# Performance work log

Hardware: AMD Instinct MI355X
Metric: run time of the kernel (lower is better)

Reference implementation:

```python
import jax, jax.numpy as jnp
import numpy as np

B, L, F = 4, 8192, 1024
H, D = 16, 64
EPS = 1e-6

def _phi(x):
    # ELU+1 positive feature map, standard for linear attention
    return jax.nn.elu(x) + 1.0

def setup_inputs() -> dict:
    key = jax.random.key(0)
    ks = jax.random.split(key, 6)
    s_in = 1.0
    s_w = 1.0 / np.sqrt(F)
    s_o = 1.0 / np.sqrt(H * D)
    return {
        "inputs_q": jax.random.normal(ks[0], (B, L, F), jnp.float32),
        "inputs_kv": jax.random.normal(ks[1], (B, L, F), jnp.float32),
        "Wq": jax.random.normal(ks[2], (F, H, D), jnp.float32) * s_w,
        "Wk": jax.random.normal(ks[3], (F, H, D), jnp.float32) * s_w,
        "Wv": jax.random.normal(ks[4], (F, H, D), jnp.float32) * s_w,
        "Wo": jax.random.normal(ks[5], (H, D, F), jnp.float32) * s_o,
    }

def reference(inputs_q, inputs_kv, Wq, Wk, Wv, Wo):
    # QKV projections (split-head kernels, no bias)
    q = jnp.einsum('bqf,fhd->bqhd', inputs_q, Wq)   # [B,Lq,H,D]
    k = jnp.einsum('bkf,fhd->bkhd', inputs_kv, Wk)  # [B,Lk,H,D]
    v = jnp.einsum('bkf,fhd->bkhd', inputs_kv, Wv)  # [B,Lk,H,D]

    qp = _phi(q)
    kp = _phi(k)

    # Linear attention: O = phi(q) @ (phi(k)^T V) / (phi(q) . sum_k phi(k))
    kv = jnp.einsum('bkhd,bkhe->bhde', kp, v)       # [B,H,D,D] small state
    ksum = jnp.sum(kp, axis=1)                       # [B,H,D]
    z = 1.0 / (jnp.einsum('bqhd,bhd->bqh', qp, ksum) + EPS)
    out = jnp.einsum('bqhd,bhde,bqh->bqhe', qp, kv, z)  # [B,Lq,H,D]

    # Output projection
    return jnp.einsum('bqhe,hef->bqf', out, Wo)      # [B,Lq,F]
```

## Files before the change

### kernel.cpp

```cpp
#include <hip/hip_runtime.h>
#include <hip/hip_fp16.h>
#include <math.h>

typedef _Float16 half8  __attribute__((ext_vector_type(8)));
typedef _Float16 half4v __attribute__((ext_vector_type(4)));
typedef float    floatx4 __attribute__((ext_vector_type(4)));

#define NB   4
#define LL   8192
#define FF   1024
#define HH   16
#define DD   64
#define MTOT 32768
#define KK   1024
#define NN   1024
#define ZSCALE 65536.0f

__device__ __forceinline__ void gload_lds16(const void* g, void* l) {
  __builtin_amdgcn_global_load_lds(
      (const __attribute__((address_space(1))) void*)g,
      (__attribute__((address_space(3))) void*)l, 16, 0, 0);
}

__device__ __forceinline__ float phi_act(float x) {
  return x > 0.f ? x + 1.f : __expf(x);
}

__global__ void k_cvt2(const float* __restrict__ a, const float* __restrict__ b,
                       _Float16* __restrict__ da, _Float16* __restrict__ db, int n4each) {
  int stride = gridDim.x * blockDim.x;
  for (int i = blockIdx.x * blockDim.x + threadIdx.x; i < 2 * n4each; i += stride) {
    const float* s; _Float16* d; int j;
    if (i < n4each) { s = a; d = da; j = i; }
    else            { s = b; d = db; j = i - n4each; }
    float4 v = reinterpret_cast<const float4*>(s)[j];
    half4v h;
    h[0] = (_Float16)v.x; h[1] = (_Float16)v.y; h[2] = (_Float16)v.z; h[3] = (_Float16)v.w;
    reinterpret_cast<half4v*>(d)[j] = h;
  }
}

__global__ void k_cvt(const float* __restrict__ src, _Float16* __restrict__ dst, int n4) {
  int stride = gridDim.x * blockDim.x;
  for (int i = blockIdx.x * blockDim.x + threadIdx.x; i < n4; i += stride) {
    float4 v = reinterpret_cast<const float4*>(src)[i];
    half4v h;
    h[0] = (_Float16)v.x; h[1] = (_Float16)v.y; h[2] = (_Float16)v.z; h[3] = (_Float16)v.w;
    reinterpret_cast<half4v*>(dst)[i] = h;
  }
}

__global__ void k_cvt_t(const float* __restrict__ W0, const float* __restrict__ W1,
                        const float* __restrict__ W2,
                        _Float16* __restrict__ T0, _Float16* __restrict__ T1,
                        _Float16* __restrict__ T2) {
  __shared__ float tile[32][33];
  int bid = blockIdx.x;
  int w = bid >> 10, rem = bid & 1023;
  int ti = rem >> 5, tj = rem & 31;
  const float* src = (w == 0) ? W0 : (w == 1) ? W1 : W2;
  _Float16*    dst = (w == 0) ? T0 : (w == 1) ? T1 : T2;
  int t = threadIdx.x;
  int r = t >> 3, c4 = (t & 7) << 2;
  float4 v = *reinterpret_cast<const float4*>(&src[(size_t)(ti * 32 + r) * FF + tj * 32 + c4]);
  tile[r][c4 + 0] = v.x; tile[r][c4 + 1] = v.y; tile[r][c4 + 2] = v.z; tile[r][c4 + 3] = v.w;
  __syncthreads();
  half4v h;
  h[0] = (_Float16)tile[c4 + 0][r];
  h[1] = (_Float16)tile[c4 + 1][r];
  h[2] = (_Float16)tile[c4 + 2][r];
  h[3] = (_Float16)tile[c4 + 3][r];
  *reinterpret_cast<half4v*>(&dst[(size_t)(tj * 32 + r) * FF + ti * 32 + c4]) = h;
}


template<int MATB, int HALF>
__device__ __forceinline__ void stage_half(const _Float16* __restrict__ G, int row0,
                                           int col0, _Float16* plane, int tid) {
  #pragma unroll
  for (int is = 0; is < 2; ++is) {
    int lin = is * 8192 + tid * 16;
    int swz = lin ^ (((lin >> 7) & 7) << 4);
    int rp = swz >> 7;
    int kb = swz & 127;
    int row;
    if constexpr (MATB) row = (rp >> 5) * 64 + HALF * 32 + (rp & 31);
    else                row = (rp >> 6) * 128 + HALF * 64 + (rp & 63);
    gload_lds16(G + (size_t)(row0 + row) * 1024 + col0 + (kb >> 1),
                (char*)plane + lin);
  }
}

__device__ __forceinline__ half8 frag_read(const _Float16* plane, int rp, int kk, int lh) {
  int byte = rp * 128 + kk * 64 + lh * 16;
  byte ^= ((byte >> 7) & 7) << 4;
  return *(const half8*)((const char*)plane + byte);
}

template<int MH, int NH>
__device__ __forceinline__ void qreads(const _Float16* sm, int buf,
                                       half8 (&bA)[8], half8 (&bB)[2][4],
                                       int wr, int wc, int lr, int lh) {
  if constexpr (NH == 0) {
    const _Float16* Ap = sm + buf * 32768 + MH * 8192;
    #pragma unroll
    for (int m = 0; m < 4; ++m)
      #pragma unroll
      for (int kk = 0; kk < 2; ++kk)
        bA[m * 2 + kk] = frag_read(Ap, wr * 64 + m * 16 + lr, kk, lh);
  }
  if constexpr (MH == 0) {
    const _Float16* Bp = sm + buf * 32768 + 16384 + NH * 8192;
    #pragma unroll
    for (int n = 0; n < 2; ++n)
      #pragma unroll
      for (int kk = 0; kk < 2; ++kk)
        bB[NH][n * 2 + kk] = frag_read(Bp, wc * 32 + n * 16 + lr, kk, lh);
  }
}

template<int MH, int NH, bool VM4>
__device__ __forceinline__ void qmfma(half8 (&bA)[8], half8 (&bB)[2][4],
                                      floatx4 (&acc)[8][4]) {
  if constexpr (VM4) {
    asm volatile("s_waitcnt vmcnt(4)" ::: "memory");
  }
  __builtin_amdgcn_s_barrier();
  __builtin_amdgcn_s_setprio(1);
  #pragma unroll
  for (int m = 0; m < 4; ++m)
    #pragma unroll
    for (int n = 0; n < 2; ++n)
      #pragma unroll
      for (int kk = 0; kk < 2; ++kk)
        acc[MH * 4 + m][NH * 2 + n] = __builtin_amdgcn_mfma_f32_16x16x32_f16(
            bA[m * 2 + kk], bB[NH][n * 2 + kk], acc[MH * 4 + m][NH * 2 + n], 0, 0, 0);
  __builtin_amdgcn_s_setprio(0);
  __builtin_amdgcn_s_barrier();
}

template<int TBUF>
__device__ __forceinline__ void do_tile(int t, const _Float16* __restrict__ Ab,
                                        const _Float16* __restrict__ Bb,
                                        int i0, int j0, _Float16* sm, int tid,
                                        half8 (&bA)[8], half8 (&bB)[2][4],
                                        floatx4 (&acc)[8][4],
                                        int wr, int wc, int lr, int lh) {
  _Float16* self  = sm + TBUF * 32768;
  _Float16* other = sm + (TBUF ^ 1) * 32768;
  const int c1 = ((t + 1 < 16) ? (t + 1) : 15) * 64;
  const int c2 = ((t + 2 < 16) ? (t + 2) : 15) * 64;
  qreads<0, 0>(sm, TBUF, bA, bB, wr, wc, lr, lh);
  stage_half<1, 1>(Bb, j0, c1, other + 24576, tid);
  qmfma<0, 0, false>(bA, bB, acc);
  qreads<0, 1>(sm, TBUF, bA, bB, wr, wc, lr, lh);
  stage_half<0, 1>(Ab, i0, c1, other + 8192, tid);
  qmfma<0, 1, false>(bA, bB, acc);
  qreads<1, 0>(sm, TBUF, bA, bB, wr, wc, lr, lh);
  stage_half<0, 0>(Ab, i0, c2, self + 0, tid);
  qmfma<1, 0, false>(bA, bB, acc);
  stage_half<1, 0>(Bb, j0, c2, self + 16384, tid);
  qmfma<1, 1, true>(bA, bB, acc);
}

template<int MODE, bool PHI>
__global__ __launch_bounds__(512, 2)
void k_gemm(const _Float16* __restrict__ A, const _Float16* __restrict__ BT,
            void* __restrict__ Cptr, float* __restrict__ aux, float outScale) {
  __shared__ __align__(16) _Float16 smem[65536];
  const int tid  = threadIdx.x;
  const int lane = tid & 63;
  const int wid  = tid >> 6;
  const int wr = wid >> 2, wc = wid & 3;
  const int lr = lane & 15, lh = lane >> 4;

  constexpr int NT = (MODE == 1) ? 8 : 4;
  constexpr int CH = (MODE == 1) ? 128 : 64;
  const int tile = (blockIdx.x & 7) * CH + (blockIdx.x >> 3);
  const int tm = tile / NT, tn = tile % NT;
  const int i0 = tm * 256, j0 = tn * 256;

  const _Float16* Ab = A;
  const _Float16* Bb = (MODE == 2) ? BT + ((size_t)(i0 >> 13)) * ((size_t)NN * KK) : BT;

  floatx4 acc[8][4];
  #pragma unroll
  for (int m = 0; m < 8; ++m)
    #pragma unroll
    for (int n = 0; n < 4; ++n)
      #pragma unroll
      for (int r = 0; r < 4; ++r) acc[m][n][r] = 0.f;

  _Float16* sm = (_Float16*)smem;
  half8 bA[8];
  half8 bB[2][4];

  stage_half<0, 0>(Ab, i0, 0,  sm + 0,             tid);
  stage_half<1, 0>(Bb, j0, 0,  sm + 16384,         tid);
  stage_half<1, 1>(Bb, j0, 0,  sm + 24576,         tid);
  stage_half<0, 1>(Ab, i0, 0,  sm + 8192,          tid);
  stage_half<0, 0>(Ab, i0, 64, sm + 32768 + 0,     tid);
  stage_half<1, 0>(Bb, j0, 64, sm + 32768 + 16384, tid);
  asm volatile("s_waitcnt vmcnt(4)" ::: "memory");
  __builtin_amdgcn_s_barrier();

  #pragma unroll 1
  for (int tt = 0; tt < 8; ++tt) {
    do_tile<0>(2 * tt,     Ab, Bb, i0, j0, sm, tid, bA, bB, acc, wr, wc, lr, lh);
    do_tile<1>(2 * tt + 1, Ab, Bb, i0, j0, sm, tid, bA, bB, acc, wr, wc, lr, lh);
  }

  asm volatile("s_waitcnt vmcnt(0)" ::: "memory");
  __builtin_amdgcn_s_barrier();

  if constexpr (MODE == 0) {
    _Float16* C = (_Float16*)Cptr;
    const int bq = i0 >> 13;
    float ks[4];
    #pragma unroll
    for (int n = 0; n < 4; ++n)
      ks[n] = aux[(size_t)bq * 1024 + j0 + wc * 64 + n * 16 + lr];
    #pragma unroll
    for (int m = 0; m < 8; ++m) {
      int row = i0 + wr * 128 + m * 16 + lh * 4;
      #pragma unroll
      for (int r = 0; r < 4; ++r) {
        float p[4];
        float dot = 0.f;
        #pragma unroll
        for (int n = 0; n < 4; ++n) {
          p[n] = phi_act(acc[m][n][r]);
          dot = fmaf(p[n], ks[n], dot);
        }
        dot += __shfl_xor(dot, 1);
        dot += __shfl_xor(dot, 2);
        dot += __shfl_xor(dot, 4);
        dot += __shfl_xor(dot, 8);
        float zf = ZSCALE / (dot + 1e-6f);
        #pragma unroll
        for (int n = 0; n < 4; ++n)
          C[(size_t)(row + r) * NN + j0 + wc * 64 + n * 16 + lr] = (_Float16)(p[n] * zf);
      }
    }
  } else if constexpr (MODE == 2) {
    float* C = (float*)Cptr;
    #pragma unroll
    for (int m = 0; m < 8; ++m) {
      int row = i0 + wr * 128 + m * 16 + lh * 4;
      #pragma unroll
      for (int n = 0; n < 4; ++n) {
        int col = j0 + wc * 64 + n * 16 + lr;
        #pragma unroll
        for (int r = 0; r < 4; ++r)
          C[(size_t)(row + r) * NN + col] = acc[m][n][r] * outScale;
      }
    }
  } else {
    const int seg = j0 >> 10;
    const int j0s = j0 & 1023;
    const int bb  = i0 >> 13;
    const int l0  = i0 & 8191;
    float s[4] = {0.f, 0.f, 0.f, 0.f};
    #pragma unroll
    for (int m = 0; m < 8; ++m) {
      int l0l = wr * 128 + m * 16 + lh * 4;
      #pragma unroll
      for (int n = 0; n < 4; ++n) {
        int n_loc = wc * 64 + n * 16 + lr;
        int byte = (n_loc * 512 + l0l * 2) ^ ((n_loc & 7) << 4);
        half4v h;
        #pragma unroll
        for (int r = 0; r < 4; ++r) {
          float v = acc[m][n][r];
          if (seg == 0) { v = phi_act(v); s[n] += v; }
          h[r] = (_Float16)v;
        }
        *(half4v*)((char*)sm + byte) = h;
      }
    }
    if (seg == 0) {
      #pragma unroll
      for (int n = 0; n < 4; ++n) {
        s[n] += __shfl_xor(s[n], 16);
        s[n] += __shfl_xor(s[n], 32);
      }
      if (lh == 0) {
        int ch = (l0 >> 7) + wr;
        size_t base = ((size_t)bb * 64 + ch) * 1024 + j0s + wc * 64 + lr;
        #pragma unroll
        for (int n = 0; n < 4; ++n) aux[base + n * 16] = s[n];
      }
    }
    __syncthreads();
    _Float16* C = (_Float16*)Cptr;
    const size_t nbase = ((size_t)seg * 4 + bb) * 1024 + j0s;
    #pragma unroll 1
    for (int pass = 0; pass < 16; ++pass) {
      int n_loc = pass * 16 + (tid >> 5);
      int lo = (tid & 31) * 16;
      int byte = (n_loc * 512 + lo) ^ ((n_loc & 7) << 4);
      half8 v = *(const half8*)((char*)sm + byte);
      *(half8*)&C[(nbase + n_loc) * LL + l0 + (lo >> 1)] = v;
    }
  }
}

__global__ void k_ksum_red(const float* __restrict__ part, float* __restrict__ ksum) {
  int i = blockIdx.x * 256 + threadIdx.x;
  int b = i >> 10, col = i & 1023;
  float s = 0.f;
  for (int c = 0; c < 64; ++c) s += part[((size_t)b * 64 + c) * 1024 + col];
  ksum[i] = s;
}

__global__ __launch_bounds__(64)
void k_stageB(const _Float16* __restrict__ kpT, const _Float16* __restrict__ vT,
              float* __restrict__ kvpart) {
  __shared__ _Float16 Ak[64 * 72];
  __shared__ _Float16 Bv[64 * 72];
  const int bid = blockIdx.x;
  const int bh = bid >> 4, cc = bid & 15;
  const int lane = threadIdx.x;
  const int lr = lane & 15, lh = lane >> 4;
  const _Float16* Ab = kpT + (size_t)bh * 64 * LL + cc * 512;
  const _Float16* Bb = vT  + (size_t)bh * 64 * LL + cc * 512;

  floatx4 acc[4][4];
  #pragma unroll
  for (int m = 0; m < 4; ++m)
    #pragma unroll
    for (int n = 0; n < 4; ++n)
      #pragma unroll
      for (int r = 0; r < 4; ++r) acc[m][n][r] = 0.f;

  for (int kt = 0; kt < 512; kt += 64) {
    __syncthreads();
    #pragma unroll
    for (int j = 0; j < 8; ++j) {
      int chunk = lane + 64 * j;
      int rr = chunk >> 3;
      int off = (chunk & 7) * 8;
      *(half8*)&Ak[rr * 72 + off] = *(const half8*)&Ab[(size_t)rr * LL + kt + off];
      *(half8*)&Bv[rr * 72 + off] = *(const half8*)&Bb[(size_t)rr * LL + kt + off];
    }
    __syncthreads();
    #pragma unroll
    for (int ks = 0; ks < 2; ++ks) {
      half8 af[4], bf[4];
      #pragma unroll
      for (int m = 0; m < 4; ++m) af[m] = *(const half8*)&Ak[(m * 16 + lr) * 72 + ks * 32 + lh * 8];
      #pragma unroll
      for (int n = 0; n < 4; ++n) bf[n] = *(const half8*)&Bv[(n * 16 + lr) * 72 + ks * 32 + lh * 8];
      #pragma unroll
      for (int m = 0; m < 4; ++m)
        #pragma unroll
        for (int n = 0; n < 4; ++n)
          acc[m][n] = __builtin_amdgcn_mfma_f32_16x16x32_f16(af[m], bf[n], acc[m][n], 0, 0, 0);
    }
  }
  float* op = kvpart + (size_t)bid * 4096;
  #pragma unroll
  for (int m = 0; m < 4; ++m)
    #pragma unroll
    for (int n = 0; n < 4; ++n)
      #pragma unroll
      for (int r = 0; r < 4; ++r)
        op[(m * 16 + lh * 4 + r) * 64 + n * 16 + lr] = acc[m][n][r];
}

__global__ void k_reduce_kv(const float* __restrict__ kvpart, float* __restrict__ kv) {
  int gid = blockIdx.x * 256 + threadIdx.x;
  int bh = gid >> 12, i = gid & 4095;
  float s = 0.f;
  for (int c = 0; c < 16; ++c) s += kvpart[((size_t)bh * 16 + c) * 4096 + i];
  kv[gid] = s;
}

__global__ __launch_bounds__(256)
void k_mker(const float* __restrict__ kv, const _Float16* __restrict__ Wo16,
            _Float16* __restrict__ MT) {
  __shared__ float kvs[4096];
  int bid = blockIdx.x;
  int fc = bid & 3, h = (bid >> 2) & 15, b = bid >> 6;
  const float* kvp = kv + ((size_t)b * 16 + h) * 4096;
  for (int i = threadIdx.x; i < 4096; i += 256) kvs[i] = kvp[i];
  __syncthreads();
  int f = fc * 256 + threadIdx.x;
  float acc[64];
  #pragma unroll
  for (int d = 0; d < 64; ++d) acc[d] = 0.f;
  for (int e = 0; e < 64; ++e) {
    float wv = (float)Wo16[(size_t)(h * 64 + e) * 1024 + f];
    #pragma unroll
    for (int d = 0; d < 64; ++d) acc[d] = fmaf(kvs[d * 64 + e], wv, acc[d]);
  }
  _Float16* op = MT + ((size_t)b * 1024 + f) * 1024 + h * 64;
  #pragma unroll
  for (int g = 0; g < 8; ++g) {
    half8 o;
    #pragma unroll
    for (int j = 0; j < 8; ++j) o[j] = (_Float16)acc[g * 8 + j];
    *(half8*)&op[g * 8] = o;
  }
}

extern "C" void kernel_launch(void* const* d_in, const int* in_sizes, int n_in,
                              void* d_out, int out_size, void* d_ws, size_t ws_size,
                              hipStream_t stream) {
  (void)in_sizes; (void)n_in; (void)out_size; (void)ws_size;
  const float* xq  = (const float*)d_in[0];
  const float* xkv = (const float*)d_in[1];
  const float* Wq  = (const float*)d_in[2];
  const float* Wk  = (const float*)d_in[3];
  const float* Wv  = (const float*)d_in[4];
  const float* Wo  = (const float*)d_in[5];

  char* ws = (char*)d_ws;
  _Float16* qp16 = (_Float16*)(ws + 0);
  _Float16* kpT  = (_Float16*)(ws + 67108864);
  _Float16* vT   = (_Float16*)(ws + 134217728);
  _Float16* WqT  = (_Float16*)(ws + 201326592);
  _Float16* WkT  = (_Float16*)(ws + 203423744);
  _Float16* WvT  = (_Float16*)(ws + 205520896);
  _Float16* Wo16 = (_Float16*)(ws + 207618048);
  float*    ksum = (float*)(ws + 209715200);
  float*    kv   = (float*)(ws + 209731584);
  float*    kvpart = (float*)(ws + 210780160);
  float*    ksum_part = (float*)(ws + 210780160);
  _Float16* MT   = (_Float16*)(ws + 227557376);

  _Float16* Xq16  = (_Float16*)d_out;
  _Float16* Xkv16 = Xq16 + 33554432;

  k_cvt2<<<4096, 256, 0, stream>>>(xq, xkv, Xq16, Xkv16, 8388608);
  k_cvt<<<512,  256, 0, stream>>>(Wo, Wo16, 262144);
  k_cvt_t<<<3072, 256, 0, stream>>>(Wq, Wk, Wv, WqT, WkT, WvT);

  k_gemm<1, false><<<1024, 512, 0, stream>>>(Xkv16, WkT, kpT, ksum_part, 1.0f);
  k_ksum_red<<<16, 256, 0, stream>>>(ksum_part, ksum);

  k_stageB<<<1024, 64, 0, stream>>>(kpT, vT, kvpart);
  k_reduce_kv<<<1024, 256, 0, stream>>>(kvpart, kv);
  k_mker<<<256, 256, 0, stream>>>(kv, Wo16, MT);

  k_gemm<0, true><<<512, 512, 0, stream>>>(Xq16, WqT, qp16, ksum, 1.0f);

  k_gemm<2, false><<<512, 512, 0, stream>>>(qp16, MT, d_out, nullptr, 1.0f / ZSCALE);
}
```

Baseline: 462.6 us.

## Fuse phi(K)^T V state computation into the KV projection GEMM epilogue

The transposed K and V weights are interleaved per head so that each 256-column GEMM tile holds phi(K) and V for two heads. The epilogue then computes per-tile partial kv states with MFMA directly from LDS, which removes the kpT/vT intermediate writes (128 MB of fp16) and the separate k_stageB kernel. The cost is more partial states to reduce (32 chunks instead of 16) and extra epilogue work and register pressure in the large GEMM.

```diff
diff --git a/kernel.cpp b/kernel.cpp
--- a/kernel.cpp
+++ b/kernel.cpp
@@ -52,14 +52,12 @@
 
 __global__ void k_cvt_t(const float* __restrict__ W0, const float* __restrict__ W1,
                         const float* __restrict__ W2,
-                        _Float16* __restrict__ T0, _Float16* __restrict__ T1,
-                        _Float16* __restrict__ T2) {
+                        _Float16* __restrict__ T0, _Float16* __restrict__ TKV) {
   __shared__ float tile[32][33];
   int bid = blockIdx.x;
   int w = bid >> 10, rem = bid & 1023;
   int ti = rem >> 5, tj = rem & 31;
   const float* src = (w == 0) ? W0 : (w == 1) ? W1 : W2;
-  _Float16*    dst = (w == 0) ? T0 : (w == 1) ? T1 : T2;
   int t = threadIdx.x;
   int r = t >> 3, c4 = (t & 7) << 2;
   float4 v = *reinterpret_cast<const float4*>(&src[(size_t)(ti * 32 + r) * FF + tj * 32 + c4]);
@@ -70,7 +68,11 @@
   h[1] = (_Float16)tile[c4 + 1][r];
   h[2] = (_Float16)tile[c4 + 2][r];
   h[3] = (_Float16)tile[c4 + 3][r];
-  *reinterpret_cast<half4v*>(&dst[(size_t)(tj * 32 + r) * FF + ti * 32 + c4]) = h;
+  int n = tj * 32 + r;
+  _Float16* dst; size_t orow;
+  if (w == 0) { dst = T0;  orow = n; }
+  else        { dst = TKV; orow = (size_t)(n >> 6) * 128 + (n & 63) + (w == 2 ? 64 : 0); }
+  *reinterpret_cast<half4v*>(&dst[orow * FF + ti * 32 + c4]) = h;
 }
 
 
@@ -166,7 +168,8 @@
 template<int MODE, bool PHI>
 __global__ __launch_bounds__(512, 2)
 void k_gemm(const _Float16* __restrict__ A, const _Float16* __restrict__ BT,
-            void* __restrict__ Cptr, float* __restrict__ aux, float outScale) {
+            void* __restrict__ Cptr, float* __restrict__ aux, float* __restrict__ aux2,
+            float outScale) {
   __shared__ __align__(16) _Float16 smem[65536];
   const int tid  = threadIdx.x;
   const int lane = tid & 63;
@@ -256,10 +259,10 @@
       }
     }
   } else {
-    const int seg = j0 >> 10;
-    const int j0s = j0 & 1023;
-    const int bb  = i0 >> 13;
-    const int l0  = i0 & 8191;
+    const int b  = i0 >> 13;
+    const int l0 = i0 & 8191;
+    const int isK = !(wc & 1);
+    const int hh  = tn * 2 + (wc >> 1);
     float s[4] = {0.f, 0.f, 0.f, 0.f};
     #pragma unroll
     for (int m = 0; m < 8; ++m) {
@@ -272,13 +275,13 @@
         #pragma unroll
         for (int r = 0; r < 4; ++r) {
           float v = acc[m][n][r];
-          if (seg == 0) { v = phi_act(v); s[n] += v; }
+          if (isK) { v = phi_act(v); s[n] += v; }
           h[r] = (_Float16)v;
         }
         *(half4v*)((char*)sm + byte) = h;
       }
     }
-    if (seg == 0) {
+    if (isK) {
       #pragma unroll
       for (int n = 0; n < 4; ++n) {
         s[n] += __shfl_xor(s[n], 16);
@@ -286,22 +289,52 @@
       }
       if (lh == 0) {
         int ch = (l0 >> 7) + wr;
-        size_t base = ((size_t)bb * 64 + ch) * 1024 + j0s + wc * 64 + lr;
+        size_t base = ((size_t)b * 64 + ch) * 1024 + (size_t)hh * 64 + lr;
         #pragma unroll
         for (int n = 0; n < 4; ++n) aux[base + n * 16] = s[n];
       }
     }
     __syncthreads();
-    _Float16* C = (_Float16*)Cptr;
-    const size_t nbase = ((size_t)seg * 4 + bb) * 1024 + j0s;
+    const int khd = wid >> 2;
+    const int db = ((wid >> 1) & 1) * 32, eb = (wid & 1) * 32;
+    const int hb = khd * 128;
+    floatx4 a2[2][2];
+    #pragma unroll
+    for (int md = 0; md < 2; ++md)
+      #pragma unroll
+      for (int ne = 0; ne < 2; ++ne)
+        #pragma unroll
+        for (int r = 0; r < 4; ++r) a2[md][ne][r] = 0.f;
     #pragma unroll 1
-    for (int pass = 0; pass < 16; ++pass) {
-      int n_loc = pass * 16 + (tid >> 5);
-      int lo = (tid & 31) * 16;
-      int byte = (n_loc * 512 + lo) ^ ((n_loc & 7) << 4);
-      half8 v = *(const half8*)((char*)sm + byte);
-      *(half8*)&C[(nbase + n_loc) * LL + l0 + (lo >> 1)] = v;
+    for (int ks2 = 0; ks2 < 8; ++ks2) {
+      half8 af[2], bf[2];
+      #pragma unroll
+      for (int md = 0; md < 2; ++md) {
+        int n_loc = hb + db + md * 16 + lr;
+        int byte = (n_loc * 512 + ks2 * 64 + lh * 16) ^ ((n_loc & 7) << 4);
+        af[md] = *(const half8*)((const char*)sm + byte);
+      }
+      #pragma unroll
+      for (int ne = 0; ne < 2; ++ne) {
+        int n_loc = hb + 64 + eb + ne * 16 + lr;
+        int byte = (n_loc * 512 + ks2 * 64 + lh * 16) ^ ((n_loc & 7) << 4);
+        bf[ne] = *(const half8*)((const char*)sm + byte);
+      }
+      #pragma unroll
+      for (int md = 0; md < 2; ++md)
+        #pragma unroll
+        for (int ne = 0; ne < 2; ++ne)
+          a2[md][ne] = __builtin_amdgcn_mfma_f32_16x16x32_f16(af[md], bf[ne], a2[md][ne], 0, 0, 0);
     }
+    const int lch = l0 >> 8;
+    float* op = aux2 + ((((size_t)b * 16 + tn * 2 + khd) * 32) + lch) * 4096;
+    #pragma unroll
+    for (int md = 0; md < 2; ++md)
+      #pragma unroll
+      for (int ne = 0; ne < 2; ++ne)
+        #pragma unroll
+        for (int r = 0; r < 4; ++r)
+          op[(db + md * 16 + lh * 4 + r) * 64 + eb + ne * 16 + lr] = a2[md][ne][r];
   }
 }
 
@@ -313,66 +346,11 @@
   ksum[i] = s;
 }
 
-__global__ __launch_bounds__(64)
-void k_stageB(const _Float16* __restrict__ kpT, const _Float16* __restrict__ vT,
-              float* __restrict__ kvpart) {
-  __shared__ _Float16 Ak[64 * 72];
-  __shared__ _Float16 Bv[64 * 72];
-  const int bid = blockIdx.x;
-  const int bh = bid >> 4, cc = bid & 15;
-  const int lane = threadIdx.x;
-  const int lr = lane & 15, lh = lane >> 4;
-  const _Float16* Ab = kpT + (size_t)bh * 64 * LL + cc * 512;
-  const _Float16* Bb = vT  + (size_t)bh * 64 * LL + cc * 512;
-
-  floatx4 acc[4][4];
-  #pragma unroll
-  for (int m = 0; m < 4; ++m)
-    #pragma unroll
-    for (int n = 0; n < 4; ++n)
-      #pragma unroll
-      for (int r = 0; r < 4; ++r) acc[m][n][r] = 0.f;
-
-  for (int kt = 0; kt < 512; kt += 64) {
-    __syncthreads();
-    #pragma unroll
-    for (int j = 0; j < 8; ++j) {
-      int chunk = lane + 64 * j;
-      int rr = chunk >> 3;
-      int off = (chunk & 7) * 8;
-      *(half8*)&Ak[rr * 72 + off] = *(const half8*)&Ab[(size_t)rr * LL + kt + off];
-      *(half8*)&Bv[rr * 72 + off] = *(const half8*)&Bb[(size_t)rr * LL + kt + off];
-    }
-    __syncthreads();
-    #pragma unroll
-    for (int ks = 0; ks < 2; ++ks) {
-      half8 af[4], bf[4];
-      #pragma unroll
-      for (int m = 0; m < 4; ++m) af[m] = *(const half8*)&Ak[(m * 16 + lr) * 72 + ks * 32 + lh * 8];
-      #pragma unroll
-      for (int n = 0; n < 4; ++n) bf[n] = *(const half8*)&Bv[(n * 16 + lr) * 72 + ks * 32 + lh * 8];
-      #pragma unroll
-      for (int m = 0; m < 4; ++m)
-        #pragma unroll
-        for (int n = 0; n < 4; ++n)
-          acc[m][n] = __builtin_amdgcn_mfma_f32_16x16x32_f16(af[m], bf[n], acc[m][n], 0, 0, 0);
-    }
-  }
-  float* op = kvpart + (size_t)bid * 4096;
-  #pragma unroll
-  for (int m = 0; m < 4; ++m)
-    #pragma unroll
-    for (int n = 0; n < 4; ++n)
-      #pragma unroll
-      for (int r = 0; r < 4; ++r)
-        op[(m * 16 + lh * 4 + r) * 64 + n * 16 + lr] = acc[m][n][r];
-}
-
 __global__ void k_reduce_kv(const float* __restrict__ kvpart, float* __restrict__ kv) {
   int gid = blockIdx.x * 256 + threadIdx.x;
   int bh = gid >> 12, i = gid & 4095;
   float s = 0.f;
-  for (int c = 0; c < 16; ++c) s += kvpart[((size_t)bh * 16 + c) * 4096 + i];
+  for (int c = 0; c < 32; ++c) s += kvpart[((size_t)bh * 32 + c) * 4096 + i];
   kv[gid] = s;
 }
 
@@ -416,34 +394,29 @@
   const float* Wo  = (const float*)d_in[5];
 
   char* ws = (char*)d_ws;
-  _Float16* qp16 = (_Float16*)(ws + 0);
-  _Float16* kpT  = (_Float16*)(ws + 67108864);
-  _Float16* vT   = (_Float16*)(ws + 134217728);
-  _Float16* WqT  = (_Float16*)(ws + 201326592);
-  _Float16* WkT  = (_Float16*)(ws + 203423744);
-  _Float16* WvT  = (_Float16*)(ws + 205520896);
-  _Float16* Wo16 = (_Float16*)(ws + 207618048);
-  float*    ksum = (float*)(ws + 209715200);
-  float*    kv   = (float*)(ws + 209731584);
-  float*    kvpart = (float*)(ws + 210780160);
-  float*    ksum_part = (float*)(ws + 210780160);
-  _Float16* MT   = (_Float16*)(ws + 227557376);
+  _Float16* qp16   = (_Float16*)(ws + 0);
+  float*    kvpart = (float*)(ws + 67108864);
+  float*    ksum_part = (float*)(ws + 100663296);
+  float*    ksum   = (float*)(ws + 101711872);
+  float*    kv     = (float*)(ws + 101728256);
+  _Float16* WqT    = (_Float16*)(ws + 102776832);
+  _Float16* WKV    = (_Float16*)(ws + 104873984);
+  _Float16* Wo16   = (_Float16*)(ws + 109068288);
+  _Float16* MT     = (_Float16*)(ws + 111165440);
 
   _Float16* Xq16  = (_Float16*)d_out;
   _Float16* Xkv16 = Xq16 + 33554432;
 
   k_cvt2<<<4096, 256, 0, stream>>>(xq, xkv, Xq16, Xkv16, 8388608);
   k_cvt<<<512,  256, 0, stream>>>(Wo, Wo16, 262144);
-  k_cvt_t<<<3072, 256, 0, stream>>>(Wq, Wk, Wv, WqT, WkT, WvT);
-
-  k_gemm<1, false><<<1024, 512, 0, stream>>>(Xkv16, WkT, kpT, ksum_part, 1.0f);
+  k_cvt_t<<<3072, 256, 0, stream>>>(Wq, Wk, Wv, WqT, WKV);
+
+  k_gemm<1, false><<<1024, 512, 0, stream>>>(Xkv16, WKV, nullptr, ksum_part, kvpart, 1.0f);
   k_ksum_red<<<16, 256, 0, stream>>>(ksum_part, ksum);
-
-  k_stageB<<<1024, 64, 0, stream>>>(kpT, vT, kvpart);
   k_reduce_kv<<<1024, 256, 0, stream>>>(kvpart, kv);
   k_mker<<<256, 256, 0, stream>>>(kv, Wo16, MT);
 
-  k_gemm<0, true><<<512, 512, 0, stream>>>(Xq16, WqT, qp16, ksum, 1.0f);
-
-  k_gemm<2, false><<<512, 512, 0, stream>>>(qp16, MT, d_out, nullptr, 1.0f / ZSCALE);
-}
+  k_gemm<0, true><<<512, 512, 0, stream>>>(Xq16, WqT, qp16, ksum, nullptr, 1.0f);
+
+  k_gemm<2, false><<<512, 512, 0, stream>>>(qp16, MT, d_out, nullptr, nullptr, 1.0f / ZSCALE);
+}
```

Result: faster. 429.8 us, median of 3 (-7.1%).
